# Kernel optimization log

Measured on AMD Instinct MI355X. Metric: run time of the kernel, lower is better.

Reference implementation:

```python
import jax, jax.numpy as jnp
import numpy as np

N = 100000   # nodes
E = 1250000  # edges per graph
D = 64       # in_feats
H = 64       # hidden_dim
C = 129      # num_classes
EPS = 1e-5


def setup_inputs() -> dict:
    key = jax.random.key(0)
    ks = jax.random.split(key, 32)
    nrm = lambda k, s: jax.random.normal(k, s, jnp.float32) * 0.05
    inp = {
        'node_features': jax.random.normal(ks[0], (N, D), jnp.float32),
        'm_src': jax.random.randint(ks[1], (E,), 0, N, jnp.int32),
        'm_dst': jax.random.randint(ks[2], (E,), 0, N, jnp.int32),
        'r_src': jax.random.randint(ks[3], (E,), 0, N, jnp.int32),
        'r_dst': jax.random.randint(ks[4], (E,), 0, N, jnp.int32),
    }
    i = 5
    for pre in ('soc', 'rt'):
        inp[pre + '_W1'] = nrm(ks[i], (D, H)); inp[pre + '_b1'] = jnp.zeros((H,), jnp.float32)
        inp[pre + '_g1'] = jnp.ones((H,), jnp.float32); inp[pre + '_bt1'] = jnp.zeros((H,), jnp.float32)
        inp[pre + '_W2'] = nrm(ks[i + 1], (H, H)); inp[pre + '_b2'] = jnp.zeros((H,), jnp.float32)
        inp[pre + '_g2'] = jnp.ones((H,), jnp.float32); inp[pre + '_bt2'] = jnp.zeros((H,), jnp.float32)
        i += 2
    inp['gW1'] = nrm(ks[i], (4 * H, H)); inp['gb1'] = jnp.zeros((H,), jnp.float32)
    inp['prelu_a'] = jnp.full((1,), 0.25, jnp.float32)
    inp['gW2'] = nrm(ks[i + 1], (H, H)); inp['gb2'] = jnp.zeros((H,), jnp.float32)
    inp['fcW'] = nrm(ks[i + 2], (H, C)); inp['fcb'] = jnp.zeros((C,), jnp.float32)
    return inp


def _gconv(h, src, dst, W, b):
    # DGL GraphConv, norm='both': D_out^{-1/2} (scatter-sum) D_in^{-1/2}, linear, ELU
    ones = jnp.ones(src.shape[0], jnp.float32)
    deg_o = jax.ops.segment_sum(ones, src, num_segments=N)
    deg_i = jax.ops.segment_sum(ones, dst, num_segments=N)
    ns = jax.lax.rsqrt(jnp.clip(deg_o, 1.0))
    nd = jax.lax.rsqrt(jnp.clip(deg_i, 1.0))
    agg = jax.ops.segment_sum((h * ns[:, None])[src], dst, num_segments=N)
    return jax.nn.elu((agg * nd[:, None]) @ W + b)


def _bn(x, g, b):
    mu = x.mean(0)
    v = x.var(0)
    return (x - mu) * jax.lax.rsqrt(v + EPS) * g + b


def _branch(x, src, dst, W1, b1, g1, bt1, W2, b2, g2, bt2):
    h = _bn(_gconv(x, src, dst, W1, b1), g1, bt1)
    return _bn(_gconv(h, src, dst, W2, b2), g2, bt2)


def reference(node_features, m_src, m_dst, r_src, r_dst,
              soc_W1, soc_b1, soc_g1, soc_bt1, soc_W2, soc_b2, soc_g2, soc_bt2,
              rt_W1, rt_b1, rt_g1, rt_bt1, rt_W2, rt_b2, rt_g2, rt_bt2,
              gW1, gb1, prelu_a, gW2, gb2, fcW, fcb):
    h1 = _branch(node_features, m_src, m_dst, soc_W1, soc_b1, soc_g1, soc_bt1, soc_W2, soc_b2, soc_g2, soc_bt2)
    h2 = _branch(node_features, r_src, r_dst, rt_W1, rt_b1, rt_g1, rt_bt1, rt_W2, rt_b2, rt_g2, rt_bt2)
    cat = jnp.concatenate([h1, h2, jnp.abs(h1 - h2), h1 * h2], axis=-1)
    z = cat @ gW1 + gb1
    z = jnp.where(z > 0, z, prelu_a * z)  # PReLU (single shared slope)
    gate = jax.nn.sigmoid(z @ gW2 + gb2)
    fused = gate * h1 + (1.0 - gate) * h2
    return fused @ fcW + fcb
```

## Files before the change

### kernel.cpp

```cpp
#include <hip/hip_runtime.h>
#include <math.h>

#define NN 100000
#define NE 1250000
#define HD 64
#define NCLS 129
#define NTILES 6250
#define GRID_T 782

#define NCHD 256
#define CHD ((NE + NCHD - 1) / NCHD)
#define NCHS 64
#define CHS ((NE + NCHS - 1) / NCHS)
#define SUBR 50000
#define NW2 12500
#define NHE (NN * (size_t)HD)

typedef float f32x4 __attribute__((ext_vector_type(4)));
typedef short bf16x8 __attribute__((ext_vector_type(8)));

__device__ __forceinline__ short f2b(float f) {
    unsigned u = __builtin_bit_cast(unsigned, f);
    u += 0x7FFFu + ((u >> 16) & 1u);
    return (short)(u >> 16);
}
__device__ __forceinline__ float b2f(short s) {
    return __builtin_bit_cast(float, ((unsigned)(unsigned short)s) << 16);
}

__global__ __launch_bounds__(1024) void k_hist8(
    const int* __restrict__ idx0, const int* __restrict__ idx1,
    unsigned char* __restrict__ P8, int chunk, int nch) {
    __shared__ unsigned int hw[NW2];
    int b = blockIdx.x, s = blockIdx.y, g = blockIdx.z;
    const int* __restrict__ idx = g ? idx1 : idx0;
    for (int i = threadIdx.x; i < NW2; i += 1024) hw[i] = 0;
    __syncthreads();
    int lo = s * SUBR;
    int beg = b * chunk, end = beg + chunk;
    if (end > NE) end = NE;
    for (int i = beg + threadIdx.x; i < end; i += 1024) {
        int v = idx[i] - lo;
        if ((unsigned)v < (unsigned)SUBR)
            atomicAdd(&hw[v >> 2], 1u << ((v & 3) * 8));
    }
    __syncthreads();
    unsigned int* dst = (unsigned int*)(P8 + ((size_t)(g * nch + b)) * NN + lo);
    for (int i = threadIdx.x; i < NW2; i += 1024) dst[i] = hw[i];
}

__global__ void k_reduce8(unsigned int* __restrict__ Pd, const unsigned int* __restrict__ Ps,
                          float* __restrict__ ns, float* __restrict__ nd,
                          int* __restrict__ degi) {
    int w = blockIdx.x * 256 + threadIdx.x;
    if (w >= NN / 4) return;
    int g = blockIdx.y;
    Pd += (size_t)g * NCHD * (NN / 4);
    Ps += (size_t)g * NCHS * (NN / 4);
    ns += (size_t)g * NN; nd += (size_t)g * NN; degi += (size_t)g * NN;
    unsigned run = 0;
#pragma unroll 8
    for (int b = 0; b < NCHD; ++b) {
        size_t o = (size_t)b * (NN / 4) + w;
        unsigned v = Pd[o];
        Pd[o] = run;
        run += v;
    }
    unsigned so = 0;
#pragma unroll 8
    for (int b = 0; b < NCHS; ++b) so += Ps[(size_t)b * (NN / 4) + w];
#pragma unroll
    for (int j = 0; j < 4; ++j) {
        int din = (run >> (8 * j)) & 255;
        int dout = (so >> (8 * j)) & 255;
        int node = w * 4 + j;
        degi[node] = din;
        ns[node] = rsqrtf((float)(dout < 1 ? 1 : dout));
        nd[node] = rsqrtf((float)(din < 1 ? 1 : din));
    }
}

__global__ void k_scan_local(const int* __restrict__ deg, int* __restrict__ excl,
                             int* __restrict__ bsums) {
    __shared__ int sm[1024];
    int g = blockIdx.y;
    deg += (size_t)g * NN; excl += (size_t)g * (NN + 1); bsums += g * 1024;
    int t = threadIdx.x;
    int i = blockIdx.x * 1024 + t;
    int v = (i < NN) ? deg[i] : 0;
    sm[t] = v;
    __syncthreads();
    for (int ofs = 1; ofs < 1024; ofs <<= 1) {
        int x = (t >= ofs) ? sm[t - ofs] : 0;
        __syncthreads();
        sm[t] += x;
        __syncthreads();
    }
    if (i < NN) excl[i] = sm[t] - v;
    if (t == 1023) bsums[blockIdx.x] = sm[1023];
}

__global__ void k_scan_tops(int* __restrict__ bsums, int nb) {
    __shared__ int sm[1024];
    bsums += blockIdx.y * 1024;
    int t = threadIdx.x;
    int v = (t < nb) ? bsums[t] : 0;
    sm[t] = v;
    __syncthreads();
    for (int ofs = 1; ofs < 1024; ofs <<= 1) {
        int x = (t >= ofs) ? sm[t - ofs] : 0;
        __syncthreads();
        sm[t] += x;
        __syncthreads();
    }
    if (t < nb) bsums[t] = sm[t] - v;
}

__global__ void k_scan_add(int* __restrict__ excl, const int* __restrict__ bsums) {
    int g = blockIdx.y;
    excl += (size_t)g * (NN + 1); bsums += g * 1024;
    int i = blockIdx.x * blockDim.x + threadIdx.x;
    if (i < NN) excl[i] += bsums[i >> 10];
    if (i == 0) excl[NN] = NE;
}

__global__ __launch_bounds__(1024) void k_fill8(
    const int* __restrict__ d0, const int* __restrict__ d1,
    const int* __restrict__ s0, const int* __restrict__ s1,
    const int* __restrict__ rowptr, const unsigned char* __restrict__ Pofs,
    int* __restrict__ col) {
    __shared__ unsigned int cur[NW2];
    int b = blockIdx.x, s = blockIdx.y, g = blockIdx.z;
    const int* __restrict__ dst = g ? d1 : d0;
    const int* __restrict__ src = g ? s1 : s0;
    rowptr += (size_t)g * (NN + 1);
    col += (size_t)g * NE;
    const unsigned char* __restrict__ ofs = Pofs + ((size_t)(g * NCHD + b)) * NN;
    for (int i = threadIdx.x; i < NW2; i += 1024) cur[i] = 0;
    __syncthreads();
    int lo = s * SUBR;
    int beg = b * CHD, end = beg + CHD;
    if (end > NE) end = NE;
    for (int i = beg + threadIdx.x; i < end; i += 1024) {
        int d = dst[i] - lo;
        if ((unsigned)d < (unsigned)SUBR) {
            unsigned old = atomicAdd(&cur[d >> 2], 1u << ((d & 3) * 8));
            int r = (old >> ((d & 3) * 8)) & 255;
            int node = d + lo;
            col[rowptr[node] + (int)ofs[node] + r] = src[i];
        }
    }
}

__global__ void k_scale_nf(const float* __restrict__ nf, const float* __restrict__ ns,
                           short* __restrict__ T) {
    int i = blockIdx.x * blockDim.x + threadIdx.x;
    if (i >= NN * 8) return;
    int g = blockIdx.y;
    ns += (size_t)g * NN; T += (size_t)g * NHE;
    int node = i >> 3;
    float s = ns[node];
    const float4* p = (const float4*)(nf + (size_t)i * 8);
    float4 a = p[0], b = p[1];
    short r[8];
    r[0] = f2b(a.x * s); r[1] = f2b(a.y * s); r[2] = f2b(a.z * s); r[3] = f2b(a.w * s);
    r[4] = f2b(b.x * s); r[5] = f2b(b.y * s); r[6] = f2b(b.z * s); r[7] = f2b(b.w * s);
    *(bf16x8*)(T + (size_t)i * 8) = *(bf16x8*)r;
}

__global__ __launch_bounds__(256) void k_gather(
    const short* __restrict__ tab, const float* __restrict__ nd,
    const int* __restrict__ rowptr, const int* __restrict__ col,
    short* __restrict__ out) {
    int w = (blockIdx.x * 256 + threadIdx.x) >> 6;
    int lane = threadIdx.x & 63;
    if (w >= NN) return;
    int g = blockIdx.y;
    tab += (size_t)g * NHE; nd += (size_t)g * NN;
    rowptr += (size_t)g * (NN + 1); col += (size_t)g * NE; out += (size_t)g * NHE;
    int beg = rowptr[w], end = rowptr[w + 1];
    float s = 0.f;
    for (int e0 = beg; e0 < end; e0 += 64) {
        int cnt = end - e0; if (cnt > 64) cnt = 64;
        int myc = (lane < cnt) ? col[e0 + lane] : 0;
        for (int j = 0; j < cnt; j += 16) {
#pragma unroll
            for (int u = 0; u < 16; ++u) {
                int c = __shfl(myc, j + u, 64);
                float v = b2f(tab[(size_t)c * HD + lane]);
                s += (j + u < cnt) ? v : 0.f;
            }
        }
    }
    out[(size_t)w * HD + lane] = f2b(s * nd[w]);
}

__global__ __launch_bounds__(256) void k_lin(
    const short* __restrict__ X, const float* __restrict__ Wa, const float* __restrict__ Wb,
    const float* __restrict__ ba, const float* __restrict__ bb,
    short* __restrict__ Y, float* __restrict__ stats) {
    __shared__ short sW[4096];
    __shared__ float sm2[128];
    int g = blockIdx.y;
    const float* W = g ? Wb : Wa;
    const float* bias = g ? bb : ba;
    X += (size_t)g * NHE; Y += (size_t)g * NHE; stats += (size_t)g * 128;
    int t = threadIdx.x;
    for (int i = t; i < 4096; i += 256) {
        int j = i & 7, l16i = (i >> 3) & 15, kgi = (i >> 7) & 3, kbi = (i >> 9) & 1, oti = (i >> 10) & 3;
        sW[i] = f2b(W[(kbi * 32 + kgi * 8 + j) * HD + oti * 16 + l16i]);
    }
    if (t < 128) sm2[t] = 0.f;
    __syncthreads();
    int lane = t & 63, wv = t >> 6, l16 = lane & 15, kg = lane >> 4;
    bf16x8 bfrag[2][4];
#pragma unroll
    for (int kb = 0; kb < 2; ++kb)
#pragma unroll
        for (int ot = 0; ot < 4; ++ot)
            bfrag[kb][ot] = *(const bf16x8*)&sW[((ot * 2 + kb) * 4 + kg) * 128 + l16 * 8];
    float bo[4];
#pragma unroll
    for (int ot = 0; ot < 4; ++ot) bo[ot] = bias[ot * 16 + l16];
    float ps[4] = {0.f, 0.f, 0.f, 0.f}, pq[4] = {0.f, 0.f, 0.f, 0.f};
    for (int tile = blockIdx.x * 4 + wv; tile < NTILES; tile += GRID_T * 4) {
        const short* xp = X + ((size_t)tile * 16 + l16) * HD + kg * 8;
        bf16x8 a0 = *(const bf16x8*)xp;
        bf16x8 a1 = *(const bf16x8*)(xp + 32);
        f32x4 acc[4];
#pragma unroll
        for (int ot = 0; ot < 4; ++ot) {
            acc[ot] = (f32x4){0.f, 0.f, 0.f, 0.f};
            acc[ot] = __builtin_amdgcn_mfma_f32_16x16x32_bf16(a0, bfrag[0][ot], acc[ot], 0, 0, 0);
            acc[ot] = __builtin_amdgcn_mfma_f32_16x16x32_bf16(a1, bfrag[1][ot], acc[ot], 0, 0, 0);
        }
#pragma unroll
        for (int ot = 0; ot < 4; ++ot) {
#pragma unroll
            for (int r = 0; r < 4; ++r) {
                float y = acc[ot][r] + bo[ot];
                y = y > 0.f ? y : expm1f(y);
                ps[ot] += y; pq[ot] += y * y;
                Y[((size_t)tile * 16 + kg * 4 + r) * HD + ot * 16 + l16] = f2b(y);
            }
        }
    }
#pragma unroll
    for (int ot = 0; ot < 4; ++ot) {
        atomicAdd(&sm2[ot * 16 + l16], ps[ot]);
        atomicAdd(&sm2[64 + ot * 16 + l16], pq[ot]);
    }
    __syncthreads();
    if (t < 128) atomicAdd(&stats[t], sm2[t]);
}

__global__ void k_bnb(const short* __restrict__ Y, short* __restrict__ O,
                      const float* __restrict__ stats,
                      const float* __restrict__ ga, const float* __restrict__ gb,
                      const float* __restrict__ bta, const float* __restrict__ btb,
                      const float* __restrict__ ns) {
    int i = blockIdx.x * blockDim.x + threadIdx.x;
    if (i >= NN * 8) return;
    int gI = blockIdx.y;
    Y += (size_t)gI * NHE; O += (size_t)gI * NHE; stats += (size_t)gI * 128;
    const float* g = gI ? gb : ga;
    const float* bt = gI ? btb : bta;
    if (ns) ns += (size_t)gI * NN;
    int node = i >> 3;
    int o0 = (i & 7) * 8;
    float extra = ns ? ns[node] : 1.f;
    bf16x8 v = *(const bf16x8*)(Y + (size_t)i * 8);
    short r[8];
    const float invN = 1.f / (float)NN;
#pragma unroll
    for (int j = 0; j < 8; ++j) {
        int o = o0 + j;
        float mu = stats[o] * invN;
        float var = fmaxf(stats[64 + o] * invN - mu * mu, 0.f);
        float isd = rsqrtf(var + 1e-5f);
        float sc = g[o] * isd * extra;
        float sh = (bt[o] - mu * g[o] * isd) * extra;
        r[j] = f2b(b2f(v[j]) * sc + sh);
    }
    *(bf16x8*)(O + (size_t)i * 8) = *(bf16x8*)r;
}

__global__ __launch_bounds__(256) void k_comb1(
    const short* __restrict__ H1, const short* __restrict__ H2,
    const float* __restrict__ W, const float* __restrict__ bias,
    const float* __restrict__ pa, short* __restrict__ Z) {
    __shared__ short sW[16384];
    int t = threadIdx.x;
    for (int i = t; i < 16384; i += 256) {
        int j = i & 7, l16i = (i >> 3) & 15, kgi = (i >> 7) & 3, kbi = (i >> 9) & 7, oti = (i >> 12) & 3;
        sW[i] = f2b(W[(kbi * 32 + kgi * 8 + j) * HD + oti * 16 + l16i]);
    }
    __syncthreads();
    int lane = t & 63, wv = t >> 6, l16 = lane & 15, kg = lane >> 4;
    float slope = pa[0];
    float bo[4];
#pragma unroll
    for (int ot = 0; ot < 4; ++ot) bo[ot] = bias[ot * 16 + l16];
    for (int tile = blockIdx.x * 4 + wv; tile < NTILES; tile += GRID_T * 4) {
        size_t rb = ((size_t)tile * 16 + l16) * HD + kg * 8;
        bf16x8 h1e = *(const bf16x8*)(H1 + rb);
        bf16x8 h1o = *(const bf16x8*)(H1 + rb + 32);
        bf16x8 h2e = *(const bf16x8*)(H2 + rb);
        bf16x8 h2o = *(const bf16x8*)(H2 + rb + 32);
        bf16x8 fe[8];
        fe[0] = h1e; fe[1] = h1o; fe[2] = h2e; fe[3] = h2o;
        short tabs[8], tprd[8];
#pragma unroll
        for (int j = 0; j < 8; ++j) {
            float a = b2f(h1e[j]), b = b2f(h2e[j]);
            tabs[j] = f2b(fabsf(a - b)); tprd[j] = f2b(a * b);
        }
        fe[4] = *(bf16x8*)tabs; fe[6] = *(bf16x8*)tprd;
#pragma unroll
        for (int j = 0; j < 8; ++j) {
            float a = b2f(h1o[j]), b = b2f(h2o[j]);
            tabs[j] = f2b(fabsf(a - b)); tprd[j] = f2b(a * b);
        }
        fe[5] = *(bf16x8*)tabs; fe[7] = *(bf16x8*)tprd;
        f32x4 acc[4];
#pragma unroll
        for (int ot = 0; ot < 4; ++ot) acc[ot] = (f32x4){0.f, 0.f, 0.f, 0.f};
#pragma unroll
        for (int kb = 0; kb < 8; ++kb)
#pragma unroll
            for (int ot = 0; ot < 4; ++ot) {
                bf16x8 bf = *(const bf16x8*)&sW[((ot * 8 + kb) * 4 + kg) * 128 + l16 * 8];
                acc[ot] = __builtin_amdgcn_mfma_f32_16x16x32_bf16(fe[kb], bf, acc[ot], 0, 0, 0);
            }
#pragma unroll
        for (int ot = 0; ot < 4; ++ot)
#pragma unroll
            for (int r = 0; r < 4; ++r) {
                float z = acc[ot][r] + bo[ot];
                z = z > 0.f ? z : slope * z;
                Z[((size_t)tile * 16 + kg * 4 + r) * HD + ot * 16 + l16] = f2b(z);
            }
    }
}

__global__ __launch_bounds__(256) void k_comb2(
    const short* __restrict__ Z, const float* __restrict__ W,
    const float* __restrict__ bias, short* __restrict__ G) {
    __shared__ short sW[4096];
    int t = threadIdx.x;
    for (int i = t; i < 4096; i += 256) {
        int j = i & 7, l16i = (i >> 3) & 15, kgi = (i >> 7) & 3, kbi = (i >> 9) & 1, oti = (i >> 10) & 3;
        sW[i] = f2b(W[(kbi * 32 + kgi * 8 + j) * HD + oti * 16 + l16i]);
    }
    __syncthreads();
    int lane = t & 63, wv = t >> 6, l16 = lane & 15, kg = lane >> 4;
    bf16x8 bfrag[2][4];
#pragma unroll
    for (int kb = 0; kb < 2; ++kb)
#pragma unroll
        for (int ot = 0; ot < 4; ++ot)
            bfrag[kb][ot] = *(const bf16x8*)&sW[((ot * 2 + kb) * 4 + kg) * 128 + l16 * 8];
    float bo[4];
#pragma unroll
    for (int ot = 0; ot < 4; ++ot) bo[ot] = bias[ot * 16 + l16];
    for (int tile = blockIdx.x * 4 + wv; tile < NTILES; tile += GRID_T * 4) {
        const short* xp = Z + ((size_t)tile * 16 + l16) * HD + kg * 8;
        bf16x8 a0 = *(const bf16x8*)xp;
        bf16x8 a1 = *(const bf16x8*)(xp + 32);
        f32x4 acc[4];
#pragma unroll
        for (int ot = 0; ot < 4; ++ot) {
            acc[ot] = (f32x4){0.f, 0.f, 0.f, 0.f};
            acc[ot] = __builtin_amdgcn_mfma_f32_16x16x32_bf16(a0, bfrag[0][ot], acc[ot], 0, 0, 0);
            acc[ot] = __builtin_amdgcn_mfma_f32_16x16x32_bf16(a1, bfrag[1][ot], acc[ot], 0, 0, 0);
        }
#pragma unroll
        for (int ot = 0; ot < 4; ++ot)
#pragma unroll
            for (int r = 0; r < 4; ++r) {
                float y = acc[ot][r] + bo[ot];
                float gate = 1.f / (1.f + expf(-y));
                G[((size_t)tile * 16 + kg * 4 + r) * HD + ot * 16 + l16] = f2b(gate);
            }
    }
}

__global__ __launch_bounds__(256) void k_fc(
    const short* __restrict__ G, const short* __restrict__ H1, const short* __restrict__ H2,
    const float* __restrict__ W, const float* __restrict__ bias,
    float* __restrict__ out) {
    __shared__ short sW[9216];
    int t = threadIdx.x;
    for (int i = t; i < 9216; i += 256) {
        int j = i & 7, l16i = (i >> 3) & 15, kgi = (i >> 7) & 3, kbi = (i >> 9) & 1, oti = i >> 10;
        int k = kbi * 32 + kgi * 8 + j, o = oti * 16 + l16i;
        sW[i] = (o < NCLS) ? f2b(W[k * NCLS + o]) : (short)0;
    }
    __syncthreads();
    int lane = t & 63, wv = t >> 6, l16 = lane & 15, kg = lane >> 4;
    float bo[9];
#pragma unroll
    for (int ot = 0; ot < 9; ++ot) {
        int o = ot * 16 + l16;
        bo[ot] = (o < NCLS) ? bias[o] : 0.f;
    }
    for (int tile = blockIdx.x * 4 + wv; tile < NTILES; tile += GRID_T * 4) {
        size_t rb = ((size_t)tile * 16 + l16) * HD;
        f32x4 acc[9];
#pragma unroll
        for (int ot = 0; ot < 9; ++ot) acc[ot] = (f32x4){0.f, 0.f, 0.f, 0.f};
#pragma unroll
        for (int kb = 0; kb < 2; ++kb) {
            int koff = kb * 32 + kg * 8;
            bf16x8 gv  = *(const bf16x8*)(G + rb + koff);
            bf16x8 h1v = *(const bf16x8*)(H1 + rb + koff);
            bf16x8 h2v = *(const bf16x8*)(H2 + rb + koff);
            short af[8];
#pragma unroll
            for (int j = 0; j < 8; ++j) {
                float gf = b2f(gv[j]);
                af[j] = f2b(gf * b2f(h1v[j]) + (1.f - gf) * b2f(h2v[j]));
            }
            bf16x8 a = *(bf16x8*)af;
#pragma unroll
            for (int ot = 0; ot < 9; ++ot) {
                bf16x8 bf = *(const bf16x8*)&sW[((ot * 2 + kb) * 4 + kg) * 128 + l16 * 8];
                acc[ot] = __builtin_amdgcn_mfma_f32_16x16x32_bf16(a, bf, acc[ot], 0, 0, 0);
            }
        }
#pragma unroll
        for (int ot = 0; ot < 9; ++ot) {
            int o = ot * 16 + l16;
            if (o < NCLS) {
#pragma unroll
                for (int r = 0; r < 4; ++r) {
                    int node = tile * 16 + kg * 4 + r;
                    out[(size_t)node * NCLS + o] = acc[ot][r] + bo[ot];
                }
            }
        }
    }
}

extern "C" void kernel_launch(void* const* d_in, const int* in_sizes, int n_in,
                              void* d_out, int out_size, void* d_ws, size_t ws_size,
                              hipStream_t stream) {
    (void)in_sizes; (void)n_in; (void)out_size; (void)ws_size;
    const int N = NN;

    const float* nf = (const float*)d_in[0];
    const int* m_src = (const int*)d_in[1];
    const int* m_dst = (const int*)d_in[2];
    const int* r_src = (const int*)d_in[3];
    const int* r_dst = (const int*)d_in[4];
    const float *W1[2], *b1[2], *g1[2], *bt1[2], *W2[2], *b2[2], *g2[2], *bt2[2];
    for (int br = 0; br < 2; ++br) {
        int base = 5 + br * 8;
        W1[br] = (const float*)d_in[base + 0];
        b1[br] = (const float*)d_in[base + 1];
        g1[br] = (const float*)d_in[base + 2];
        bt1[br] = (const float*)d_in[base + 3];
        W2[br] = (const float*)d_in[base + 4];
        b2[br] = (const float*)d_in[base + 5];
        g2[br] = (const float*)d_in[base + 6];
        bt2[br] = (const float*)d_in[base + 7];
    }
    const float* gW1 = (const float*)d_in[21];
    const float* gb1 = (const float*)d_in[22];
    const float* pa  = (const float*)d_in[23];
    const float* gW2 = (const float*)d_in[24];
    const float* gb2 = (const float*)d_in[25];
    const float* fcW = (const float*)d_in[26];
    const float* fcb = (const float*)d_in[27];
    float* out = (float*)d_out;

    char* p = (char*)d_ws;
    auto take = [&](size_t bytes) { char* r = p; p += (bytes + 255) & ~(size_t)255; return r; };
    size_t NHb = (size_t)N * HD * 2;
    unsigned char* P8d = (unsigned char*)take((size_t)2 * NCHD * NN);
    unsigned char* P8s = (unsigned char*)take((size_t)2 * NCHS * NN);
    short* T   = (short*)take(2 * NHb);
    short* X   = (short*)take(2 * NHb);
    short* Y   = (short*)take(2 * NHb);
    short* Hs  = (short*)take(2 * NHb);
    short* H   = (short*)take(2 * NHb);
    float* ns = (float*)take((size_t)2 * N * 4);
    float* nd = (float*)take((size_t)2 * N * 4);
    float* stats = (float*)take(2 * 2 * 128 * 4);
    int* degi = (int*)take((size_t)2 * N * 4);
    int* rowptr = (int*)take((size_t)2 * (N + 1) * 4);
    int* bsums = (int*)take(2 * 4096);
    short* Z = (short*)d_out;
    int* col = (int*)((char*)d_out + NHb);

    int gN = (N + 255) / 256;
    int nScanBlk = (N + 1023) / 1024;
    int gEW = (N * 8 + 255) / 256;
    int gW4 = (N / 4 + 255) / 256;
    int gGat = (N * 64) / 256;

    k_hist8<<<dim3(NCHD, 2, 2), 1024, 0, stream>>>(m_dst, r_dst, P8d, CHD, NCHD);
    k_hist8<<<dim3(NCHS, 2, 2), 1024, 0, stream>>>(m_src, r_src, P8s, CHS, NCHS);
    k_reduce8<<<dim3(gW4, 2), 256, 0, stream>>>((unsigned int*)P8d, (const unsigned int*)P8s,
                                                ns, nd, degi);
    k_scan_local<<<dim3(nScanBlk, 2), 1024, 0, stream>>>(degi, rowptr, bsums);
    k_scan_tops<<<dim3(1, 2), 1024, 0, stream>>>(bsums, nScanBlk);
    k_scan_add<<<dim3(gN, 2), 256, 0, stream>>>(rowptr, bsums);
    k_fill8<<<dim3(NCHD, 2, 2), 1024, 0, stream>>>(m_dst, r_dst, m_src, r_src, rowptr, P8d, col);
    hipMemsetAsync(stats, 0, 2 * 2 * 128 * 4, stream);

    k_scale_nf<<<dim3(gEW, 2), 256, 0, stream>>>(nf, ns, T);
    k_gather<<<dim3(gGat, 2), 256, 0, stream>>>(T, nd, rowptr, col, X);
    k_lin<<<dim3(GRID_T, 2), 256, 0, stream>>>(X, W1[0], W1[1], b1[0], b1[1], Y, stats);
    k_bnb<<<dim3(gEW, 2), 256, 0, stream>>>(Y, Hs, stats, g1[0], g1[1], bt1[0], bt1[1], ns);

    k_gather<<<dim3(gGat, 2), 256, 0, stream>>>(Hs, nd, rowptr, col, X);
    k_lin<<<dim3(GRID_T, 2), 256, 0, stream>>>(X, W2[0], W2[1], b2[0], b2[1], Y, stats + 256);
    k_bnb<<<dim3(gEW, 2), 256, 0, stream>>>(Y, H, stats + 256, g2[0], g2[1], bt2[0], bt2[1],
                                            (const float*)nullptr);

    k_comb1<<<GRID_T, 256, 0, stream>>>(H, H + NHb / 2, gW1, gb1, pa, Z);
    k_comb2<<<GRID_T, 256, 0, stream>>>(Z, gW2, gb2, X);
    k_fc<<<GRID_T, 256, 0, stream>>>(X, H, H + NHb / 2, fcW, fcb, out);
}
```

Before: 459.5 us.

## Vectorize gather with 4-edge-per-wave lanes and zero sentinel row

The CSR gather kernel now has each quarter-wave handle a different edge, and each lane loads 4 bf16 values (8 bytes) instead of one 2-byte value. Partial sums are combined with cross-lane xor shuffles. A zeroed sentinel row at index NN is appended to every feature table so padded edge slots read zeros, which removes the per-element predicate. This cuts the number of load instructions per edge and widens memory transactions, at the cost of one extra row per buffer and a few more shuffles per node.

```diff
diff --git a/kernel.cpp b/kernel.cpp
--- a/kernel.cpp
+++ b/kernel.cpp
@@ -14,7 +14,7 @@
 #define CHS ((NE + NCHS - 1) / NCHS)
 #define SUBR 50000
 #define NW2 12500
-#define NHE (NN * (size_t)HD)
+#define NHE2 ((NN + 1) * (size_t)HD)
 
 typedef float f32x4 __attribute__((ext_vector_type(4)));
 typedef short bf16x8 __attribute__((ext_vector_type(8)));
@@ -155,16 +155,21 @@
 __global__ void k_scale_nf(const float* __restrict__ nf, const float* __restrict__ ns,
                            short* __restrict__ T) {
     int i = blockIdx.x * blockDim.x + threadIdx.x;
-    if (i >= NN * 8) return;
+    if (i >= (NN + 1) * 8) return;
     int g = blockIdx.y;
-    ns += (size_t)g * NN; T += (size_t)g * NHE;
+    ns += (size_t)g * NN; T += (size_t)g * NHE2;
     int node = i >> 3;
-    float s = ns[node];
-    const float4* p = (const float4*)(nf + (size_t)i * 8);
-    float4 a = p[0], b = p[1];
     short r[8];
-    r[0] = f2b(a.x * s); r[1] = f2b(a.y * s); r[2] = f2b(a.z * s); r[3] = f2b(a.w * s);
-    r[4] = f2b(b.x * s); r[5] = f2b(b.y * s); r[6] = f2b(b.z * s); r[7] = f2b(b.w * s);
+    if (node == NN) {
+#pragma unroll
+        for (int j = 0; j < 8; ++j) r[j] = 0;
+    } else {
+        float s = ns[node];
+        const float4* p = (const float4*)(nf + (size_t)i * 8);
+        float4 a = p[0], b = p[1];
+        r[0] = f2b(a.x * s); r[1] = f2b(a.y * s); r[2] = f2b(a.z * s); r[3] = f2b(a.w * s);
+        r[4] = f2b(b.x * s); r[5] = f2b(b.y * s); r[6] = f2b(b.z * s); r[7] = f2b(b.w * s);
+    }
     *(bf16x8*)(T + (size_t)i * 8) = *(bf16x8*)r;
 }
 
@@ -176,23 +181,40 @@
     int lane = threadIdx.x & 63;
     if (w >= NN) return;
     int g = blockIdx.y;
-    tab += (size_t)g * NHE; nd += (size_t)g * NN;
-    rowptr += (size_t)g * (NN + 1); col += (size_t)g * NE; out += (size_t)g * NHE;
+    tab += (size_t)g * NHE2; nd += (size_t)g * NN;
+    rowptr += (size_t)g * (NN + 1); col += (size_t)g * NE; out += (size_t)g * NHE2;
+    int grp = lane >> 4;
+    int sub = lane & 15;
     int beg = rowptr[w], end = rowptr[w + 1];
-    float s = 0.f;
+    float a0 = 0.f, a1 = 0.f, a2 = 0.f, a3 = 0.f;
     for (int e0 = beg; e0 < end; e0 += 64) {
         int cnt = end - e0; if (cnt > 64) cnt = 64;
-        int myc = (lane < cnt) ? col[e0 + lane] : 0;
+        int myc = (lane < cnt) ? col[e0 + lane] : NN;
         for (int j = 0; j < cnt; j += 16) {
 #pragma unroll
-            for (int u = 0; u < 16; ++u) {
-                int c = __shfl(myc, j + u, 64);
-                float v = b2f(tab[(size_t)c * HD + lane]);
-                s += (j + u < cnt) ? v : 0.f;
-            }
-        }
-    }
-    out[(size_t)w * HD + lane] = f2b(s * nd[w]);
+            for (int u = 0; u < 4; ++u) {
+                int c = __shfl(myc, j + u * 4 + grp, 64);
+                uint2 v = *(const uint2*)(tab + (size_t)c * HD + sub * 4);
+                a0 += __builtin_bit_cast(float, v.x << 16);
+                a1 += __builtin_bit_cast(float, v.x & 0xffff0000u);
+                a2 += __builtin_bit_cast(float, v.y << 16);
+                a3 += __builtin_bit_cast(float, v.y & 0xffff0000u);
+            }
+        }
+    }
+    a0 += __shfl_xor(a0, 16, 64); a1 += __shfl_xor(a1, 16, 64);
+    a2 += __shfl_xor(a2, 16, 64); a3 += __shfl_xor(a3, 16, 64);
+    a0 += __shfl_xor(a0, 32, 64); a1 += __shfl_xor(a1, 32, 64);
+    a2 += __shfl_xor(a2, 32, 64); a3 += __shfl_xor(a3, 32, 64);
+    if (grp == 0) {
+        float s = nd[w];
+        unsigned r0 = ((unsigned)(unsigned short)f2b(a0 * s)) |
+                      (((unsigned)(unsigned short)f2b(a1 * s)) << 16);
+        unsigned r1 = ((unsigned)(unsigned short)f2b(a2 * s)) |
+                      (((unsigned)(unsigned short)f2b(a3 * s)) << 16);
+        uint2 r; r.x = r0; r.y = r1;
+        *(uint2*)(out + (size_t)w * HD + sub * 4) = r;
+    }
 }
 
 __global__ __launch_bounds__(256) void k_lin(
@@ -204,7 +226,7 @@
     int g = blockIdx.y;
     const float* W = g ? Wb : Wa;
     const float* bias = g ? bb : ba;
-    X += (size_t)g * NHE; Y += (size_t)g * NHE; stats += (size_t)g * 128;
+    X += (size_t)g * NHE2; Y += (size_t)g * NHE2; stats += (size_t)g * 128;
     int t = threadIdx.x;
     for (int i = t; i < 4096; i += 256) {
         int j = i & 7, l16i = (i >> 3) & 15, kgi = (i >> 7) & 3, kbi = (i >> 9) & 1, oti = (i >> 10) & 3;
@@ -260,27 +282,32 @@
                       const float* __restrict__ bta, const float* __restrict__ btb,
                       const float* __restrict__ ns) {
     int i = blockIdx.x * blockDim.x + threadIdx.x;
-    if (i >= NN * 8) return;
+    if (i >= (NN + 1) * 8) return;
     int gI = blockIdx.y;
-    Y += (size_t)gI * NHE; O += (size_t)gI * NHE; stats += (size_t)gI * 128;
+    Y += (size_t)gI * NHE2; O += (size_t)gI * NHE2; stats += (size_t)gI * 128;
     const float* g = gI ? gb : ga;
     const float* bt = gI ? btb : bta;
     if (ns) ns += (size_t)gI * NN;
     int node = i >> 3;
-    int o0 = (i & 7) * 8;
-    float extra = ns ? ns[node] : 1.f;
-    bf16x8 v = *(const bf16x8*)(Y + (size_t)i * 8);
     short r[8];
-    const float invN = 1.f / (float)NN;
-#pragma unroll
-    for (int j = 0; j < 8; ++j) {
-        int o = o0 + j;
-        float mu = stats[o] * invN;
-        float var = fmaxf(stats[64 + o] * invN - mu * mu, 0.f);
-        float isd = rsqrtf(var + 1e-5f);
-        float sc = g[o] * isd * extra;
-        float sh = (bt[o] - mu * g[o] * isd) * extra;
-        r[j] = f2b(b2f(v[j]) * sc + sh);
+    if (node == NN) {
+#pragma unroll
+        for (int j = 0; j < 8; ++j) r[j] = 0;
+    } else {
+        int o0 = (i & 7) * 8;
+        float extra = ns ? ns[node] : 1.f;
+        bf16x8 v = *(const bf16x8*)(Y + (size_t)i * 8);
+        const float invN = 1.f / (float)NN;
+#pragma unroll
+        for (int j = 0; j < 8; ++j) {
+            int o = o0 + j;
+            float mu = stats[o] * invN;
+            float var = fmaxf(stats[64 + o] * invN - mu * mu, 0.f);
+            float isd = rsqrtf(var + 1e-5f);
+            float sc = g[o] * isd * extra;
+            float sh = (bt[o] - mu * g[o] * isd) * extra;
+            r[j] = f2b(b2f(v[j]) * sc + sh);
+        }
     }
     *(bf16x8*)(O + (size_t)i * 8) = *(bf16x8*)r;
 }
@@ -476,14 +503,14 @@
 
     char* p = (char*)d_ws;
     auto take = [&](size_t bytes) { char* r = p; p += (bytes + 255) & ~(size_t)255; return r; };
-    size_t NHb = (size_t)N * HD * 2;
+    size_t NHb2 = NHE2 * 2;
     unsigned char* P8d = (unsigned char*)take((size_t)2 * NCHD * NN);
     unsigned char* P8s = (unsigned char*)take((size_t)2 * NCHS * NN);
-    short* T   = (short*)take(2 * NHb);
-    short* X   = (short*)take(2 * NHb);
-    short* Y   = (short*)take(2 * NHb);
-    short* Hs  = (short*)take(2 * NHb);
-    short* H   = (short*)take(2 * NHb);
+    short* T   = (short*)take(2 * NHb2);
+    short* X   = (short*)take(2 * NHb2);
+    short* Y   = (short*)take(2 * NHb2);
+    short* Hs  = (short*)take(2 * NHb2);
+    short* H   = (short*)take(2 * NHb2);
     float* ns = (float*)take((size_t)2 * N * 4);
     float* nd = (float*)take((size_t)2 * N * 4);
     float* stats = (float*)take(2 * 2 * 128 * 4);
@@ -491,11 +518,11 @@
     int* rowptr = (int*)take((size_t)2 * (N + 1) * 4);
     int* bsums = (int*)take(2 * 4096);
     short* Z = (short*)d_out;
-    int* col = (int*)((char*)d_out + NHb);
+    int* col = (int*)((char*)d_out + (size_t)N * HD * 2);
 
     int gN = (N + 255) / 256;
     int nScanBlk = (N + 1023) / 1024;
-    int gEW = (N * 8 + 255) / 256;
+    int gEW = ((N + 1) * 8 + 255) / 256;
     int gW4 = (N / 4 + 255) / 256;
     int gGat = (N * 64) / 256;
 
@@ -519,7 +546,7 @@
     k_bnb<<<dim3(gEW, 2), 256, 0, stream>>>(Y, H, stats + 256, g2[0], g2[1], bt2[0], bt2[1],
                                             (const float*)nullptr);
 
-    k_comb1<<<GRID_T, 256, 0, stream>>>(H, H + NHb / 2, gW1, gb1, pa, Z);
+    k_comb1<<<GRID_T, 256, 0, stream>>>(H, H + NHE2, gW1, gb1, pa, Z);
     k_comb2<<<GRID_T, 256, 0, stream>>>(Z, gW2, gb2, X);
-    k_fc<<<GRID_T, 256, 0, stream>>>(X, H, H + NHb / 2, fcW, fcb, out);
-}
+    k_fc<<<GRID_T, 256, 0, stream>>>(X, H, H + NHE2, fcW, fcb, out);
+}
```

Measured after the change: 446.0 us. 1.03x faster.
